# Optimization experiments

Hardware: AMD Instinct MI355X
Metric: run time of the kernel (lower is better)

The kernel has to match this reference:

```python
import jax, jax.numpy as jnp
import numpy as np

# Static config (matches init_kwargs)
B = 1
D = 1024          # model_dim
H = 16            # num_heads
HD = 64           # head_dim
TPF = 256         # tokens_per_frame = latent_height*latent_width
LH, LW = 16, 16
FRAMES = 13
PREFIX = 1
ATTN = 3
CHUNKS = 4
TXT = 226                 # text_length per chunk
SEQ_TXT = CHUNKS * TXT    # 904
VID_LEN = FRAMES * TPF    # 3328
CHUNK_VID = (PREFIX + ATTN) * TPF  # 1024 video tokens per attention chunk
THETA = 10000.0
EPS = 1e-6
SCALE = 1.0 / np.sqrt(HD)
DT, DHE, DW = 16, 24, 24  # 3D rope split of head_dim


def setup_inputs() -> dict:
    key = jax.random.key(0)
    ks = jax.random.split(key, 16)
    def w(k, shape, s=0.02):
        return (jax.random.normal(k, shape) * s).astype(jnp.float32)
    return dict(
        vid_emb=jax.random.normal(ks[0], (B, VID_LEN, D), jnp.float32),
        text_emb=jax.random.normal(ks[1], (B, SEQ_TXT, D), jnp.float32),
        Wq=w(ks[2], (D, D)), bq=jnp.zeros((D,), jnp.float32),
        Wk=w(ks[3], (D, D)), bk=jnp.zeros((D,), jnp.float32),
        Wv=w(ks[4], (D, D)), bv=jnp.zeros((D,), jnp.float32),
        Wo=w(ks[5], (D, D)), bo=jnp.zeros((D,), jnp.float32),
        qn_w=jnp.ones((HD,), jnp.float32), qn_b=jnp.zeros((HD,), jnp.float32),
        kn_w=jnp.ones((HD,), jnp.float32), kn_b=jnp.zeros((HD,), jnp.float32),
        ssm_Win=w(ks[6], (D, D)), ssm_Wout=w(ks[7], (D, D)),
        ssm_gate=jnp.zeros((D,), jnp.float32),
        fg_t=jnp.full((D,), 0.1, jnp.float32), fg_v=jnp.full((D,), 0.1, jnp.float32),
        bg_t=jnp.full((D,), 0.1, jnp.float32), bg_v=jnp.full((D,), 0.1, jnp.float32),
    )


def _layernorm(x, w, b):
    mu = jnp.mean(x, axis=-1, keepdims=True)
    var = jnp.mean((x - mu) ** 2, axis=-1, keepdims=True)
    return (x - mu) * jax.lax.rsqrt(var + EPS) * w + b


def _rope_angles():
    # per-video-token 3D positions within a chunk
    tok = jnp.arange(CHUNK_VID)
    f = (tok // TPF).astype(jnp.float32)
    rem = tok % TPF
    hp = (rem // LW).astype(jnp.float32)
    wp = (rem % LW).astype(jnp.float32)
    def inv(d):
        return THETA ** (-jnp.arange(0, d, 2, dtype=jnp.float32) / d)
    return f[:, None] * inv(DT), hp[:, None] * inv(DHE), wp[:, None] * inv(DW)


def _rot(x, ang):
    half = x.shape[-1] // 2
    c, s = jnp.cos(ang), jnp.sin(ang)
    x1, x2 = x[..., :half], x[..., half:]
    return jnp.concatenate([x1 * c - x2 * s, x1 * s + x2 * c], axis=-1)


def _apply_rope3d(x, angs):
    at, ah, aw = angs
    return jnp.concatenate([
        _rot(x[..., :DT], at),
        _rot(x[..., DT:DT + DHE], ah),
        _rot(x[..., DT + DHE:], aw),
    ], axis=-1)


def _attn_forward(vid_emb, text_emb, Wq, bq, Wk, bk, Wv, bv, Wo, bo, qn_w, qn_b, kn_w, kn_b):
    b = vid_emb.shape[0]
    starts = np.arange(CHUNKS) * ATTN * TPF
    idx = jnp.asarray(starts)[:, None] + jnp.arange(CHUNK_VID)[None, :]  # [C, CHUNK_VID]
    txt_chunks = text_emb.reshape(b, CHUNKS, TXT, D)
    vid_chunks = vid_emb[:, idx]                                          # [b, C, CHUNK_VID, D]
    cur = jnp.concatenate([txt_chunks, vid_chunks], axis=2)               # [b, C, T, D]
    T = TXT + CHUNK_VID
    cur = cur.reshape(b * CHUNKS, T, D)

    def heads(x):
        return x.reshape(b * CHUNKS, T, H, HD).transpose(0, 2, 1, 3)      # [bc, h, t, d]

    q = _layernorm(heads(cur @ Wq + bq), qn_w, qn_b)
    k = _layernorm(heads(cur @ Wk + bk), kn_w, kn_b)
    v = heads(cur @ Wv + bv)

    angs = _rope_angles()
    q = jnp.concatenate([q[:, :, :TXT], _apply_rope3d(q[:, :, TXT:], angs)], axis=2)
    k = jnp.concatenate([k[:, :, :TXT], _apply_rope3d(k[:, :, TXT:], angs)], axis=2)

    scores = jnp.einsum('bhqd,bhkd->bhqk', q, k) * SCALE
    attn = jax.nn.softmax(scores, axis=-1)
    out = jnp.einsum('bhqk,bhkd->bhqd', attn, v)
    out = out.transpose(0, 2, 1, 3).reshape(b * CHUNKS, T, D) @ Wo + bo
    out = out.reshape(b, CHUNKS, T, D)

    text_out = out[:, :, :TXT].reshape(b, SEQ_TXT, D)
    vid_part = out[:, :, TXT:]                                            # [b, C, CHUNK_VID, D]
    vid_acc = jnp.zeros((b, VID_LEN, D), vid_emb.dtype).at[:, idx].add(vid_part)
    cnt = jnp.zeros((b, VID_LEN, 1), vid_emb.dtype).at[:, idx].add(jnp.ones((b, CHUNKS, CHUNK_VID, 1), vid_emb.dtype))
    vid_out = vid_acc / cnt
    return jnp.concatenate([text_out, vid_out], axis=1)


def _ssm(x, Win, Wout, gate_logit):
    # simplified TTT stand-in: gated linear recurrence h_t = g*h_{t-1} + u_t (causal scan)
    g = jax.nn.sigmoid(gate_logit)
    u = x @ Win
    a = jnp.broadcast_to(g, u.shape)
    def comb(c1, c2):
        a1, b1 = c1
        a2, b2 = c2
        return a1 * a2, a2 * b1 + b2
    _, h = jax.lax.associative_scan(comb, (a, u), axis=1)
    return h @ Wout


def _rev_text_chunks(t):
    b = t.shape[0]
    return jnp.flip(t.reshape(b, CHUNKS, TXT, D), axis=1).reshape(b, SEQ_TXT, D)


def _ssm_forward(emb, ssm_Win, ssm_Wout, ssm_gate, fg_t, fg_v, bg_t, bg_v):
    Ttxt = SEQ_TXT
    res = emb
    y = _ssm(emb, ssm_Win, ssm_Wout, ssm_gate)
    emb = res + jnp.concatenate([jnp.tanh(fg_t) * y[:, :Ttxt], jnp.tanh(fg_v) * y[:, Ttxt:]], axis=1)
    res2 = emb
    # multiscene reverse: flip text chunk order and video token order
    rev = jnp.concatenate([_rev_text_chunks(emb[:, :Ttxt]), jnp.flip(emb[:, Ttxt:], axis=1)], axis=1)
    y2 = _ssm(rev, ssm_Win, ssm_Wout, ssm_gate)
    y2 = jnp.concatenate([_rev_text_chunks(y2[:, :Ttxt]), jnp.flip(y2[:, Ttxt:], axis=1)], axis=1)
    return res2 + jnp.concatenate([jnp.tanh(bg_t) * y2[:, :Ttxt], jnp.tanh(bg_v) * y2[:, Ttxt:]], axis=1)


def reference(vid_emb, text_emb, Wq, bq, Wk, bk, Wv, bv, Wo, bo, qn_w, qn_b, kn_w, kn_b,
              ssm_Win, ssm_Wout, ssm_gate, fg_t, fg_v, bg_t, bg_v):
    emb = _attn_forward(vid_emb, text_emb, Wq, bq, Wk, bk, Wv, bv, Wo, bo, qn_w, qn_b, kn_w, kn_b)
    out = _ssm_forward(emb, ssm_Win, ssm_Wout, ssm_gate, fg_t, fg_v, bg_t, bg_v)
    return out[:, SEQ_TXT:], out[:, :SEQ_TXT]
```

## Files before the change

kernel.cpp:

```cpp
#include <hip/hip_runtime.h>
#include <cstdint>

constexpr int Dm       = 1024;
constexpr int Hh       = 16;
constexpr int HD       = 64;
constexpr int CHUNKS   = 4;
constexpr int TXT      = 226;
constexpr int SEQ_TXT  = 904;
constexpr int VID_LEN  = 3328;
constexpr int CHUNK_VID= 1024;
constexpr int Tt       = 1250;
constexpr int Tp       = 1280;
constexpr int M_QKV    = 5000;
constexpr int SEQm     = 4232;
constexpr int STRIDE_V = 768;
constexpr float EPSc   = 1e-6f;
constexpr float SCALEc = 0.125f;
constexpr float OFFS   = 8.0f;
constexpr float C16    = 1.6609640474f;
constexpr float C24    = 1.1073093649f;

constexpr int SEGL2 = 64;
constexpr int HALO  = 64;
constexpr int NSEG2 = (SEQm + SEGL2 - 1) / SEGL2;

typedef __attribute__((ext_vector_type(8))) short bf16x8;
typedef __attribute__((ext_vector_type(4))) float f32x4;

__device__ __forceinline__ ushort f2bf(float x) {
    uint32_t u = __float_as_uint(x);
    u += 0x7FFFu + ((u >> 16) & 1u);
    return (ushort)(u >> 16);
}
__device__ __forceinline__ float bf2f(ushort b) {
    return __uint_as_float(((uint32_t)b) << 16);
}

__device__ __forceinline__ void gload_lds16(const ushort* g, ushort* l) {
    __builtin_amdgcn_global_load_lds(
        (const __attribute__((address_space(1))) unsigned int*)g,
        (__attribute__((address_space(3))) unsigned int*)l, 16, 0, 0);
}

__device__ __forceinline__ int rev_map(int i) {
    if (i < SEQ_TXT) {
        int c = i / TXT, o = i - c * TXT;
        return (CHUNKS - 1 - c) * TXT + o;
    }
    int j = i - SEQ_TXT;
    return SEQ_TXT + (VID_LEN - 1 - j);
}

__global__ __launch_bounds__(256) void prep_all(
    const float* __restrict__ Wq, const float* __restrict__ Wk,
    const float* __restrict__ Wv, const float* __restrict__ Wo,
    const float* __restrict__ Win, const float* __restrict__ Wout,
    const float* __restrict__ vid, const float* __restrict__ txt,
    ushort* __restrict__ WqkvH, ushort* __restrict__ WqkvL,
    ushort* __restrict__ WoH, ushort* __restrict__ WoL,
    ushort* __restrict__ WinH, ushort* __restrict__ WinL,
    ushort* __restrict__ WoutH, ushort* __restrict__ WoutL,
    ushort* __restrict__ chi, ushort* __restrict__ clo) {
    __shared__ float tile[32][33];
    if (blockIdx.z == 6) {
        int base = (blockIdx.y * 32 + blockIdx.x) * 256 + threadIdx.x;
        for (int idx = base; idx < M_QKV * 256; idx += 32 * 32 * 256) {
            int row = idx >> 8, c4 = (idx & 255) * 4;
            int c = row / Tt, t = row - c * Tt;
            float4 x;
            if (t < TXT)
                x = *(const float4*)(txt + (size_t)(c * TXT + t) * Dm + c4);
            else
                x = *(const float4*)(vid + (size_t)(c * STRIDE_V + (t - TXT)) * Dm + c4);
            float v[4] = {x.x, x.y, x.z, x.w};
            ushort4 h, l;
            h.x = f2bf(v[0]); l.x = f2bf(v[0] - bf2f(h.x));
            h.y = f2bf(v[1]); l.y = f2bf(v[1] - bf2f(h.y));
            h.z = f2bf(v[2]); l.z = f2bf(v[2] - bf2f(h.z));
            h.w = f2bf(v[3]); l.w = f2bf(v[3] - bf2f(h.w));
            *(ushort4*)(chi + (size_t)row * Dm + c4) = h;
            *(ushort4*)(clo + (size_t)row * Dm + c4) = l;
        }
        return;
    }
    const float* W; ushort* Thi; ushort* Tlo;
    switch (blockIdx.z) {
        case 0: W = Wq;  Thi = WqkvH;               Tlo = WqkvL;               break;
        case 1: W = Wk;  Thi = WqkvH + 1024*1024;   Tlo = WqkvL + 1024*1024;   break;
        case 2: W = Wv;  Thi = WqkvH + 2*1024*1024; Tlo = WqkvL + 2*1024*1024; break;
        case 3: W = Wo;  Thi = WoH;   Tlo = WoL;   break;
        case 4: W = Win; Thi = WinH;  Tlo = WinL;  break;
        default:W = Wout;Thi = WoutH; Tlo = WoutL; break;
    }
    int k0 = blockIdx.y * 32, n0 = blockIdx.x * 32;
    int j = threadIdx.x & 31, i0 = threadIdx.x >> 5;
#pragma unroll
    for (int i = i0; i < 32; i += 8)
        tile[i][j] = W[(size_t)(k0 + i) * 1024 + n0 + j];
    __syncthreads();
#pragma unroll
    for (int i = i0; i < 32; i += 8) {
        float v = tile[j][i];
        ushort h = f2bf(v);
        size_t o = (size_t)(n0 + i) * 1024 + k0 + j;
        Thi[o] = h;
        Tlo[o] = f2bf(v - bf2f(h));
    }
}

template<int MODE>
__global__ __launch_bounds__(256) void gemm_sk(
    const ushort* __restrict__ Ahi, const ushort* __restrict__ Alo,
    const ushort* __restrict__ Bhi, const ushort* __restrict__ Blo,
    const float* __restrict__ f1, const float* __restrict__ f2,
    const float* __restrict__ f3,
    float* __restrict__ Cf, ushort* __restrict__ u1,
    int M, int N) {
    __shared__ ushort AHL[128 * 64];
    __shared__ ushort BHL[128 * 64];
    const int tid = threadIdx.x;
    const int w = tid >> 6, lane = tid & 63;
    const int lrow = lane & 15, quad = lane >> 4;
    const int mBase = blockIdx.y * 128, nBase = blockIdx.x * 128;

    const bool isB = (w >= 2);
    const int half = w & 1;
    const ushort* Phi = isB ? Bhi : Ahi;
    const ushort* Plo = isB ? Blo : Alo;
    ushort* lds = (isB ? BHL : AHL) + half * 4096;
    const int baseR = (isB ? nBase : mBase) + half * 64;
    const int maxr = (isB ? N : M) - 1;
    const int rl8 = lane >> 3;
    const int c = (lane & 7) ^ rl8;
    const ushort* Psel = (c < 4) ? Phi : Plo;
    const ushort* gb[8];
#pragma unroll
    for (int u = 0; u < 8; ++u) {
        int rg = min(baseR + u * 8 + rl8, maxr);
        gb[u] = Psel + (size_t)rg * 1024 + (c & 3) * 8;
    }

    const int mo = (w >> 1) * 64, no = (w & 1) * 64;
    const int p = quad ^ (lrow & 7);
    f32x4 acc[4][4];
#pragma unroll
    for (int i = 0; i < 4; ++i)
#pragma unroll
        for (int j = 0; j < 4; ++j) acc[i][j] = (f32x4){0.f, 0.f, 0.f, 0.f};

    const int kk0 = (MODE == 5) ? blockIdx.z * 512 : 0;
    const int kk1 = (MODE == 5) ? kk0 + 512 : 1024;
    for (int kk = kk0; kk < kk1; kk += 32) {
        __syncthreads();
#pragma unroll
        for (int u = 0; u < 8; ++u) gload_lds16(gb[u] + kk, lds + u * 512);
        __syncthreads();

        bf16x8 ah[4], al[4], bh[4], bl[4];
#pragma unroll
        for (int i = 0; i < 4; ++i) {
            int m = mo + i * 16 + lrow;
            ah[i] = *(const bf16x8*)&AHL[m * 64 + p * 8];
            al[i] = *(const bf16x8*)&AHL[m * 64 + (p ^ 4) * 8];
        }
#pragma unroll
        for (int j = 0; j < 4; ++j) {
            int n = no + j * 16 + lrow;
            bh[j] = *(const bf16x8*)&BHL[n * 64 + p * 8];
            bl[j] = *(const bf16x8*)&BHL[n * 64 + (p ^ 4) * 8];
        }
#pragma unroll
        for (int i = 0; i < 4; ++i)
#pragma unroll
            for (int j = 0; j < 4; ++j) {
                f32x4 a = acc[i][j];
                a = __builtin_amdgcn_mfma_f32_16x16x32_bf16(ah[i], bh[j], a, 0, 0, 0);
                a = __builtin_amdgcn_mfma_f32_16x16x32_bf16(al[i], bh[j], a, 0, 0, 0);
                a = __builtin_amdgcn_mfma_f32_16x16x32_bf16(ah[i], bl[j], a, 0, 0, 0);
                acc[i][j] = a;
            }
    }

    const size_t zoff = (MODE == 5) ? (size_t)blockIdx.z * M * N : 0;
#pragma unroll
    for (int i = 0; i < 4; ++i)
#pragma unroll
        for (int j = 0; j < 4; ++j) {
            const int col = nBase + no + j * 16 + lrow;
            float bv = 0.f;
            if constexpr (MODE == 1)
                bv = (col < 1024) ? f1[col]
                   : (col < 2048) ? f2[col - 1024] : f3[col - 2048];
#pragma unroll
            for (int r = 0; r < 4; ++r) {
                const int row = mBase + mo + i * 16 + quad * 4 + r;
                if (row >= M) continue;
                const size_t idx = (size_t)row * N + col;
                const float a = acc[i][j][r];
                if constexpr (MODE == 1) {
                    u1[idx] = f2bf(a + bv);
                } else {
                    Cf[zoff + idx] = a;
                }
            }
        }
}

__global__ __launch_bounds__(512, 2) void gemm_qkv_8ph(
    const ushort* __restrict__ Ahi, const ushort* __restrict__ Alo,
    const ushort* __restrict__ Bhi, const ushort* __restrict__ Blo,
    const float* __restrict__ f1, const float* __restrict__ f2,
    const float* __restrict__ f3, ushort* __restrict__ out) {
    constexpr int Mq  = M_QKV;
    constexpr int Nq  = 3072;
    constexpr int NSL = 32;

    __shared__ __align__(16) ushort ldsq[65536];

    const int tid = threadIdx.x;
    const int w = tid >> 6, lane = tid & 63;
    const int lrow = lane & 15, quad = lane >> 4;
    const int wr = w >> 2, wc = w & 3;
    const int mBase = blockIdx.y * 256, nBase = blockIdx.x * 256;

    const int cA = (tid & 7) ^ ((tid >> 3) & 7);
    const ushort* pA = (cA < 4) ? Ahi : Alo;
    const ushort* pB = (cA < 4) ? Bhi : Blo;
    uint32_t offA[4], offB[4];
#pragma unroll
    for (int q = 0; q < 4; ++q) {
        const int r = q * 64 + (tid >> 3);
        offA[q] = (uint32_t)(min(mBase + r, Mq - 1) * 1024 + (cA & 3) * 8);
        offB[q] = (uint32_t)((nBase + r) * 1024 + (cA & 3) * 8);
    }
    const int ldsW = w * 512;

    const int pH = quad ^ (lrow & 7);
    const int arow = wr * 128 + lrow;
    const int brow = wc * 64 + lrow;

    f32x4 acc[8][4];
#pragma unroll
    for (int i = 0; i < 8; ++i)
#pragma unroll
        for (int j = 0; j < 4; ++j) acc[i][j] = (f32x4){0.f, 0.f, 0.f, 0.f};

#define STAGE_AB(b, s) do { \
        ushort* dA_ = ldsq + (b) * 16384 + ldsW; \
        ushort* dB_ = ldsq + 32768 + (b) * 16384 + ldsW; \
        const uint32_t ko_ = (uint32_t)(s) * 32u; \
        gload_lds16(pA + offA[0] + ko_, dA_); \
        gload_lds16(pA + offA[1] + ko_, dA_ + 4096); \
        gload_lds16(pA + offA[2] + ko_, dA_ + 8192); \
        gload_lds16(pA + offA[3] + ko_, dA_ + 12288); \
        gload_lds16(pB + offB[0] + ko_, dB_); \
        gload_lds16(pB + offB[1] + ko_, dB_ + 4096); \
        gload_lds16(pB + offB[2] + ko_, dB_ + 8192); \
        gload_lds16(pB + offB[3] + ko_, dB_ + 12288); \
    } while (0)

    STAGE_AB(0, 0);
    asm volatile("s_waitcnt vmcnt(0)" ::: "memory");
    __builtin_amdgcn_s_barrier();

#pragma unroll 1
    for (int s = 0; s < NSL; ++s) {
        const int b = s & 1;
        if (s + 1 < NSL) STAGE_AB(1 - b, s + 1);

        const ushort* aB_ = ldsq + b * 16384;
        const ushort* bB_ = ldsq + 32768 + b * 16384;
        bf16x8 ahi[8], alo[8], bhi[4], blo[4];
#pragma unroll
        for (int i = 0; i < 8; ++i) {
            const ushort* rp = aB_ + (arow + i * 16) * 64;
            ahi[i] = *(const bf16x8*)(rp + pH * 8);
            alo[i] = *(const bf16x8*)(rp + (pH ^ 4) * 8);
        }
#pragma unroll
        for (int j = 0; j < 4; ++j) {
            const ushort* rp = bB_ + (brow + j * 16) * 64;
            bhi[j] = *(const bf16x8*)(rp + pH * 8);
            blo[j] = *(const bf16x8*)(rp + (pH ^ 4) * 8);
        }

        __builtin_amdgcn_s_barrier();
        asm volatile("s_waitcnt lgkmcnt(0)" ::: "memory");
        __builtin_amdgcn_s_setprio(1);
#pragma unroll
        for (int i = 0; i < 8; ++i)
#pragma unroll
            for (int j = 0; j < 4; ++j) {
                f32x4 a = acc[i][j];
                a = __builtin_amdgcn_mfma_f32_16x16x32_bf16(ahi[i], bhi[j], a, 0, 0, 0);
                a = __builtin_amdgcn_mfma_f32_16x16x32_bf16(alo[i], bhi[j], a, 0, 0, 0);
                a = __builtin_amdgcn_mfma_f32_16x16x32_bf16(ahi[i], blo[j], a, 0, 0, 0);
                acc[i][j] = a;
            }
        __builtin_amdgcn_s_setprio(0);
        asm volatile("s_waitcnt vmcnt(0)" ::: "memory");
        __builtin_amdgcn_s_barrier();
    }

#undef STAGE_AB

#pragma unroll
    for (int i = 0; i < 8; ++i) {
#pragma unroll
        for (int j = 0; j < 4; ++j) {
            const int col = nBase + wc * 64 + j * 16 + lrow;
            const float bias = (col < 1024) ? f1[col]
                             : (col < 2048) ? f2[col - 1024] : f3[col - 2048];
#pragma unroll
            for (int r = 0; r < 4; ++r) {
                const int row = mBase + wr * 128 + i * 16 + quad * 4 + r;
                if (row < Mq)
                    out[(size_t)row * Nq + col] = f2bf(acc[i][j][r] + bias);
            }
        }
    }
}

__global__ __launch_bounds__(256) void lnrope(
    const ushort* __restrict__ qkvb,
    const float* __restrict__ qn_w, const float* __restrict__ qn_b,
    const float* __restrict__ kn_w, const float* __restrict__ kn_b,
    ushort* __restrict__ qP, ushort* __restrict__ kP, ushort* __restrict__ vT) {
    __shared__ ushort vtile[64][72];
    const int ch = blockIdx.y, c = ch >> 4, h = ch & 15;
    const int t0 = blockIdx.x * 64;
    const int tid = threadIdx.x, w = tid >> 6, lane = tid & 63;

    auto wsum = [](float x) {
#pragma unroll
        for (int o = 32; o; o >>= 1) x += __shfl_xor(x, o);
        return x;
    };

#pragma unroll 1
    for (int it = 0; it < 16; ++it) {
        const int tl = w * 16 + it;
        const int t = t0 + tl;
        ushort qb = 0, kb = 0, vb = 0;
        if (t < Tt) {
            size_t src = (size_t)(c * Tt + t) * 3072 + h * HD + lane;
            float qv = bf2f(qkvb[src]);
            float kv = bf2f(qkvb[src + 1024]);
            float vv = bf2f(qkvb[src + 2048]);

            float qmu = wsum(qv) * (1.f / 64.f);
            float qd  = qv - qmu;
            float qvar = wsum(qd * qd) * (1.f / 64.f);
            float qn = qd * rsqrtf(qvar + EPSc) * qn_w[lane] + qn_b[lane];

            float kmu = wsum(kv) * (1.f / 64.f);
            float kd  = kv - kmu;
            float kvar = wsum(kd * kd) * (1.f / 64.f);
            float kn = kd * rsqrtf(kvar + EPSc) * kn_w[lane] + kn_b[lane];

            if (t >= TXT) {
                int pos = t - TXT;
                int f = pos >> 8, rem2 = pos & 255, hp = rem2 >> 4, wp = rem2 & 15;
                int p, dl; float cc;
                if (lane < 16)      { cc = C16; p = f;  dl = lane; }
                else if (lane < 40) { cc = C24; p = hp; dl = lane - 16; }
                else                { cc = C24; p = wp; dl = lane - 40; }
                int halfd = (lane < 16) ? 8 : 12;
                int i = (dl < halfd) ? dl : dl - halfd;
                float ang = (float)p * exp2f(-(float)i * cc);
                float cs = cosf(ang), sn = sinf(ang);
                int partner = (dl < halfd) ? (lane + halfd) : (lane - halfd);
                float qo = __shfl(qn, partner);
                float ko = __shfl(kn, partner);
                qn = (dl < halfd) ? (qn * cs - qo * sn) : (qo * sn + qn * cs);
                kn = (dl < halfd) ? (kn * cs - ko * sn) : (ko * sn + kn * cs);
            }
            qb = f2bf(qn * SCALEc);
            kb = f2bf(kn);
            vb = f2bf(vv);
        }
        size_t dst = ((size_t)ch * Tp + t) * HD + lane;
        qP[dst] = qb;
        kP[dst] = kb;
        vtile[tl][lane] = vb;
    }
    __syncthreads();
    const int r = tid >> 2, ck = tid & 3;
    ushort* dst = vT + ((size_t)ch * HD + r) * Tp + t0;
    short o1[8], o2[8];
#pragma unroll
    for (int j = 0; j < 8; ++j) {
        o1[j] = (short)vtile[ck * 8 + j][r];
        o2[j] = (short)vtile[(ck + 4) * 8 + j][r];
    }
    *(bf16x8*)(dst + ck * 8)       = *(bf16x8*)o1;
    *(bf16x8*)(dst + (ck + 4) * 8) = *(bf16x8*)o2;
}

__global__ __launch_bounds__(256) void attn_mfma(
    const ushort* __restrict__ qP, const ushort* __restrict__ kP,
    const ushort* __restrict__ vT,
    ushort* __restrict__ ohi, ushort* __restrict__ olo) {
    const int ch = blockIdx.y;
    const int c = ch >> 4, h = ch & 15;
    const int qbase = blockIdx.x * 64;
    const int tid = threadIdx.x, w = tid >> 6, lane = tid & 63;
    const int lrow = lane & 15, quad = lane >> 4;

    __shared__ ushort KT[2][32 * 64];
    __shared__ ushort VTs[2][64 * 32];
    __shared__ ushort PB[4][16][40];

    const ushort* kg = kP + (size_t)ch * Tp * HD;
    const ushort* vg = vT + (size_t)ch * HD * Tp;

    const ushort* kgl = kg + (size_t)(w * 8 + (lane >> 3)) * HD
                           + ((lane & 7) ^ ((lane >> 3) & 7)) * 8;
    const ushort* vgl = vg + (size_t)(w * 16 + (lane >> 2)) * Tp + (lane & 3) * 8;

    const int qr = qbase + w * 16 + lrow;
    const ushort* qgp = qP + ((size_t)ch * Tp + qr) * HD + quad * 8;
    bf16x8 qf0 = *(const bf16x8*)qgp;
    bf16x8 qf1 = *(const bf16x8*)(qgp + 32);

    f32x4 accO[4];
#pragma unroll
    for (int dt = 0; dt < 4; ++dt) accO[dt] = (f32x4){0.f, 0.f, 0.f, 0.f};
    float lacc[4] = {0.f, 0.f, 0.f, 0.f};

    gload_lds16(kgl, &KT[0][w * 512]);
    gload_lds16(vgl, &VTs[0][w * 512]);

    const int NSTEP = Tp / 32;
    for (int s = 0; s < NSTEP; ++s) {
        const int b = s & 1;
        __syncthreads();
        if (s + 1 < NSTEP) {
            int kb = (s + 1) * 32;
            gload_lds16(kgl + (size_t)kb * HD, &KT[1 - b][w * 512]);
            gload_lds16(vgl + kb, &VTs[1 - b][w * 512]);
        }

        const int sw = lrow & 7;
        const ushort* r0 = &KT[b][lrow * 64];
        const ushort* r1 = &KT[b][(16 + lrow) * 64];
        bf16x8 k00 = *(const bf16x8*)(r0 + (quad ^ sw) * 8);
        bf16x8 k01 = *(const bf16x8*)(r0 + ((4 + quad) ^ sw) * 8);
        bf16x8 k10 = *(const bf16x8*)(r1 + (quad ^ sw) * 8);
        bf16x8 k11 = *(const bf16x8*)(r1 + ((4 + quad) ^ sw) * 8);
        f32x4 s0 = (f32x4){0.f, 0.f, 0.f, 0.f}, s1 = s0;
        s0 = __builtin_amdgcn_mfma_f32_16x16x32_bf16(qf0, k00, s0, 0, 0, 0);
        s0 = __builtin_amdgcn_mfma_f32_16x16x32_bf16(qf1, k01, s0, 0, 0, 0);
        s1 = __builtin_amdgcn_mfma_f32_16x16x32_bf16(qf0, k10, s1, 0, 0, 0);
        s1 = __builtin_amdgcn_mfma_f32_16x16x32_bf16(qf1, k11, s1, 0, 0, 0);

#pragma unroll
        for (int r = 0; r < 4; ++r) {
            float p0 = __expf(s0[r] - OFFS);
            float p1 = __expf(s1[r] - OFFS);
            lacc[r] += p0 + p1;
            int row = quad * 4 + r;
            PB[w][row][lrow]      = f2bf(p0);
            PB[w][row][16 + lrow] = f2bf(p1);
        }

        bf16x8 pf = *(const bf16x8*)&PB[w][lrow][quad * 8];
#pragma unroll
        for (int dt = 0; dt < 4; ++dt) {
            bf16x8 vf = *(const bf16x8*)&VTs[b][(dt * 16 + lrow) * 32 + quad * 8];
            accO[dt] = __builtin_amdgcn_mfma_f32_16x16x32_bf16(pf, vf, accO[dt], 0, 0, 0);
        }
    }

    float il[4];
#pragma unroll
    for (int r = 0; r < 4; ++r) {
        float l = lacc[r];
        l += __shfl_xor(l, 1);
        l += __shfl_xor(l, 2);
        l += __shfl_xor(l, 4);
        l += __shfl_xor(l, 8);
        l -= (float)(Tp - Tt) * __expf(-OFFS);
        il[r] = 1.f / l;
    }
#pragma unroll
    for (int dt = 0; dt < 4; ++dt)
#pragma unroll
        for (int r = 0; r < 4; ++r) {
            int qrow = qbase + w * 16 + quad * 4 + r;
            if (qrow < Tt) {
                float val = accO[dt][r] * il[r];
                size_t o = (size_t)(c * Tt + qrow) * Dm + h * HD + dt * 16 + lrow;
                ushort hv = f2bf(val);
                ohi[o] = hv;
                olo[o] = f2bf(val - bf2f(hv));
            }
        }
}

__global__ __launch_bounds__(256) void reduce_scatter(
    const float* __restrict__ P0, const float* __restrict__ bo,
    ushort* __restrict__ ehi, ushort* __restrict__ elo) {
    const float* P1 = P0 + (size_t)M_QKV * Dm;
    int idx = blockIdx.x * 256 + threadIdx.x;
    int row = idx >> 8, c4 = (idx & 255) * 4;
    float sx, sy, sz, sw;
    if (row < SEQ_TXT) {
        int c = row / TXT, t = row - c * TXT;
        size_t o = (size_t)(c * Tt + t) * Dm + c4;
        float4 a = *(const float4*)(P0 + o);
        float4 b = *(const float4*)(P1 + o);
        sx = a.x + b.x; sy = a.y + b.y; sz = a.z + b.z; sw = a.w + b.w;
    } else {
        int p = row - SEQ_TXT;
        sx = sy = sz = sw = 0.f; int cnt = 0;
#pragma unroll
        for (int c = 0; c < CHUNKS; ++c) {
            int off = p - c * STRIDE_V;
            if (off >= 0 && off < CHUNK_VID) {
                size_t o = (size_t)(c * Tt + TXT + off) * Dm + c4;
                float4 a = *(const float4*)(P0 + o);
                float4 b = *(const float4*)(P1 + o);
                sx += a.x + b.x; sy += a.y + b.y;
                sz += a.z + b.z; sw += a.w + b.w;
                ++cnt;
            }
        }
        float inv = 1.f / (float)cnt;
        sx *= inv; sy *= inv; sz *= inv; sw *= inv;
    }
    float4 b4 = *(const float4*)(bo + c4);
    float v[4] = {sx + b4.x, sy + b4.y, sz + b4.z, sw + b4.w};
    ushort4 h, l;
    h.x = f2bf(v[0]); l.x = f2bf(v[0] - bf2f(h.x));
    h.y = f2bf(v[1]); l.y = f2bf(v[1] - bf2f(h.y));
    h.z = f2bf(v[2]); l.z = f2bf(v[2] - bf2f(h.z));
    h.w = f2bf(v[3]); l.w = f2bf(v[3] - bf2f(h.w));
    *(ushort4*)(ehi + (size_t)row * Dm + c4) = h;
    *(ushort4*)(elo + (size_t)row * Dm + c4) = l;
}

__global__ __launch_bounds__(256) void scan_halo(
    const float* __restrict__ P0, const float* __restrict__ gate,
    ushort* __restrict__ hhi, ushort* __restrict__ hlo, int perm) {
    const float* P1 = P0 + (size_t)SEQm * Dm;
    int ch = blockIdx.x * 256 + threadIdx.x;
    int seg = blockIdx.y;
    float g = 1.f / (1.f + expf(-gate[ch]));
    int tw0 = seg * SEGL2;
    int tw1 = min(SEQm, tw0 + SEGL2);
    int t0 = max(0, tw0 - HALO);
    float hv = 0.f;
    for (int t = t0; t < tw0; ++t) {
        int rt = perm ? rev_map(t) : t;
        size_t o = (size_t)rt * Dm + ch;
        hv = fmaf(g, hv, P0[o] + P1[o]);
    }
    for (int t = tw0; t < tw1; ++t) {
        int rt = perm ? rev_map(t) : t;
        size_t o = (size_t)rt * Dm + ch;
        hv = fmaf(g, hv, P0[o] + P1[o]);
        ushort h = f2bf(hv);
        hhi[o] = h;
        hlo[o] = f2bf(hv - bf2f(h));
    }
}

__global__ __launch_bounds__(256) void reduce_c1(
    const float* __restrict__ P0,
    const ushort* __restrict__ ehi, const ushort* __restrict__ elo,
    const float* __restrict__ fg_t, const float* __restrict__ fg_v,
    float* __restrict__ emb2, ushort* __restrict__ e2hi, ushort* __restrict__ e2lo) {
    const float* P1 = P0 + (size_t)SEQm * Dm;
    int idx = blockIdx.x * 256 + threadIdx.x;
    int row = idx >> 8, c4 = (idx & 255) * 4;
    const float* fg = (row < SEQ_TXT) ? fg_t : fg_v;
    size_t o = (size_t)row * Dm + c4;
    float4 a = *(const float4*)(P0 + o);
    float4 b = *(const float4*)(P1 + o);
    ushort4 eh = *(const ushort4*)(ehi + o);
    ushort4 el = *(const ushort4*)(elo + o);
    float v[4];
    v[0] = (bf2f(eh.x) + bf2f(el.x)) + tanhf(fg[c4 + 0]) * (a.x + b.x);
    v[1] = (bf2f(eh.y) + bf2f(el.y)) + tanhf(fg[c4 + 1]) * (a.y + b.y);
    v[2] = (bf2f(eh.z) + bf2f(el.z)) + tanhf(fg[c4 + 2]) * (a.z + b.z);
    v[3] = (bf2f(eh.w) + bf2f(el.w)) + tanhf(fg[c4 + 3]) * (a.w + b.w);
    *(float4*)(emb2 + o) = make_float4(v[0], v[1], v[2], v[3]);
    ushort4 h, l;
    h.x = f2bf(v[0]); l.x = f2bf(v[0] - bf2f(h.x));
    h.y = f2bf(v[1]); l.y = f2bf(v[1] - bf2f(h.y));
    h.z = f2bf(v[2]); l.z = f2bf(v[2] - bf2f(h.z));
    h.w = f2bf(v[3]); l.w = f2bf(v[3] - bf2f(h.w));
    *(ushort4*)(e2hi + o) = h;
    *(ushort4*)(e2lo + o) = l;
}

__global__ __launch_bounds__(256) void reduce_fin(
    const float* __restrict__ P0, const float* __restrict__ emb2,
    const float* __restrict__ bg_t, const float* __restrict__ bg_v,
    float* __restrict__ outp) {
    const float* P1 = P0 + (size_t)SEQm * Dm;
    int idx = blockIdx.x * 256 + threadIdx.x;
    int row = idx >> 8, c4 = (idx & 255) * 4;
    const float* bg = (row < SEQ_TXT) ? bg_t : bg_v;
    int drow = (row >= SEQ_TXT) ? (row - SEQ_TXT) : (VID_LEN + row);
    size_t o = (size_t)row * Dm + c4;
    float4 a = *(const float4*)(P0 + o);
    float4 b = *(const float4*)(P1 + o);
    float4 e = *(const float4*)(emb2 + o);
    float4 r = make_float4(e.x + tanhf(bg[c4 + 0]) * (a.x + b.x),
                           e.y + tanhf(bg[c4 + 1]) * (a.y + b.y),
                           e.z + tanhf(bg[c4 + 2]) * (a.z + b.z),
                           e.w + tanhf(bg[c4 + 3]) * (a.w + b.w));
    *(float4*)(outp + (size_t)drow * Dm + c4) = r;
}

extern "C" void kernel_launch(void* const* d_in, const int* in_sizes, int n_in,
                              void* d_out, int out_size, void* d_ws, size_t ws_size,
                              hipStream_t stream) {
    const float* vid_emb = (const float*)d_in[0];
    const float* text_emb= (const float*)d_in[1];
    const float* Wq = (const float*)d_in[2];  const float* bq = (const float*)d_in[3];
    const float* Wk = (const float*)d_in[4];  const float* bk = (const float*)d_in[5];
    const float* Wv = (const float*)d_in[6];  const float* bv = (const float*)d_in[7];
    const float* Wo = (const float*)d_in[8];  const float* bo = (const float*)d_in[9];
    const float* qn_w = (const float*)d_in[10]; const float* qn_b = (const float*)d_in[11];
    const float* kn_w = (const float*)d_in[12]; const float* kn_b = (const float*)d_in[13];
    const float* Win  = (const float*)d_in[14]; const float* Wout = (const float*)d_in[15];
    const float* gate = (const float*)d_in[16];
    const float* fg_t = (const float*)d_in[17]; const float* fg_v = (const float*)d_in[18];
    const float* bg_t = (const float*)d_in[19]; const float* bg_v = (const float*)d_in[20];

    char* W8 = (char*)d_ws;
    if (ws_size < 128647168u) return;
    ushort* WqkvH = (ushort*)(W8 + 0);
    ushort* WqkvL = (ushort*)(W8 + 6291456);
    ushort* WoH   = (ushort*)(W8 + 12582912);
    ushort* WoL   = (ushort*)(W8 + 14680064);
    ushort* WinH  = (ushort*)(W8 + 16777216);
    ushort* WinL  = (ushort*)(W8 + 18874368);
    ushort* WoutH = (ushort*)(W8 + 20971520);
    ushort* WoutL = (ushort*)(W8 + 23068672);
    ushort* qkvb  = (ushort*)(W8 + 25165824);
    ushort* curH  = (ushort*)(W8 + 55885824);
    ushort* curL  = (ushort*)(W8 + 66125824);
    ushort* qPl   = (ushort*)(W8 + 76365824);
    ushort* kPl   = (ushort*)(W8 + 86851584);
    ushort* vTl   = (ushort*)(W8 + 97337344);
    ushort* aoutH = (ushort*)(W8 + 25165824);
    ushort* aoutL = (ushort*)(W8 + 35405824);
    float*  PWo   = (float*) (W8 + 76365824);
    ushort* embH  = (ushort*)(W8 + 45645824);
    ushort* embL  = (ushort*)(W8 + 54312960);
    float*  PW    = (float*) (W8 + 76365824);
    ushort* hbufH = (ushort*)(W8 + 25165824);
    ushort* hbufL = (ushort*)(W8 + 33832960);
    float*  emb2  = (float*) (W8 + 111034368);
    ushort* e2H   = (ushort*)(W8 + 25165824);
    ushort* e2L   = (ushort*)(W8 + 33832960);
    ushort* hbuf2H= (ushort*)(W8 + 45645824);
    ushort* hbuf2L= (ushort*)(W8 + 54312960);
    float*  outp  = (float*)d_out;

    prep_all<<<dim3(32, 32, 7), 256, 0, stream>>>(
        Wq, Wk, Wv, Wo, Win, Wout, vid_emb, text_emb,
        WqkvH, WqkvL, WoH, WoL, WinH, WinL, WoutH, WoutL, curH, curL);

    gemm_qkv_8ph<<<dim3(12, 20), 512, 0, stream>>>(
        curH, curL, WqkvH, WqkvL, bq, bk, bv, qkvb);

    lnrope<<<dim3(Tp / 64, 64), 256, 0, stream>>>(qkvb, qn_w, qn_b, kn_w, kn_b,
                                                  qPl, kPl, vTl);

    attn_mfma<<<dim3(Tp / 64, 64), 256, 0, stream>>>(qPl, kPl, vTl, aoutH, aoutL);

    gemm_sk<5><<<dim3(8, 40, 2), 256, 0, stream>>>(
        aoutH, aoutL, WoH, WoL, nullptr, nullptr, nullptr, PWo, nullptr,
        M_QKV, 1024);
    reduce_scatter<<<SEQm, 256, 0, stream>>>(PWo, bo, embH, embL);

    dim3 gsq(8, 34, 2);
    dim3 gscan(Dm / 256, NSEG2);

    gemm_sk<5><<<gsq, 256, 0, stream>>>(
        embH, embL, WinH, WinL, nullptr, nullptr, nullptr, PW, nullptr,
        SEQm, 1024);
    scan_halo<<<gscan, 256, 0, stream>>>(PW, gate, hbufH, hbufL, 0);
    gemm_sk<5><<<gsq, 256, 0, stream>>>(
        hbufH, hbufL, WoutH, WoutL, nullptr, nullptr, nullptr, PW, nullptr,
        SEQm, 1024);
    reduce_c1<<<SEQm, 256, 0, stream>>>(PW, embH, embL, fg_t, fg_v,
                                        emb2, e2H, e2L);

    gemm_sk<5><<<gsq, 256, 0, stream>>>(
        e2H, e2L, WinH, WinL, nullptr, nullptr, nullptr, PW, nullptr,
        SEQm, 1024);
    scan_halo<<<gscan, 256, 0, stream>>>(PW, gate, hbuf2H, hbuf2L, 1);
    gemm_sk<5><<<gsq, 256, 0, stream>>>(
        hbuf2H, hbuf2L, WoutH, WoutL, nullptr, nullptr, nullptr, PW, nullptr,
        SEQm, 1024);
    reduce_fin<<<SEQm, 256, 0, stream>>>(PW, emb2, bg_t, bg_v, outp);
}
```

Before: 656.5 us.

## Double-buffer LDS tiles in split-bf16 GEMM to overlap loads with MFMA

Doubles the LDS staging buffers in the gemm_sk kernel so the next k-slice is fetched directly into LDS while MFMAs run on the current slice. This replaces the two barriers per iteration with one wait-and-barrier at the end. It also raises wave priority around the MFMA block. LDS use doubles to 64 KB per block, which may cut occupancy.

```diff
diff --git a/kernel.cpp b/kernel.cpp
--- a/kernel.cpp
+++ b/kernel.cpp
@@ -116,8 +116,8 @@
     const float* __restrict__ f3,
     float* __restrict__ Cf, ushort* __restrict__ u1,
     int M, int N) {
-    __shared__ ushort AHL[128 * 64];
-    __shared__ ushort BHL[128 * 64];
+    __shared__ ushort AHL[2][128 * 64];
+    __shared__ ushort BHL[2][128 * 64];
     const int tid = threadIdx.x;
     const int w = tid >> 6, lane = tid & 63;
     const int lrow = lane & 15, quad = lane >> 4;
@@ -127,7 +127,8 @@
     const int half = w & 1;
     const ushort* Phi = isB ? Bhi : Ahi;
     const ushort* Plo = isB ? Blo : Alo;
-    ushort* lds = (isB ? BHL : AHL) + half * 4096;
+    ushort* st0 = (isB ? BHL[0] : AHL[0]) + half * 4096;
+    ushort* st1 = (isB ? BHL[1] : AHL[1]) + half * 4096;
     const int baseR = (isB ? nBase : mBase) + half * 64;
     const int maxr = (isB ? N : M) - 1;
     const int rl8 = lane >> 3;
@@ -150,25 +151,37 @@
 
     const int kk0 = (MODE == 5) ? blockIdx.z * 512 : 0;
     const int kk1 = (MODE == 5) ? kk0 + 512 : 1024;
-    for (int kk = kk0; kk < kk1; kk += 32) {
-        __syncthreads();
-#pragma unroll
-        for (int u = 0; u < 8; ++u) gload_lds16(gb[u] + kk, lds + u * 512);
-        __syncthreads();
-
+
+#pragma unroll
+    for (int u = 0; u < 8; ++u) gload_lds16(gb[u] + kk0, st0 + u * 512);
+    asm volatile("s_waitcnt vmcnt(0)" ::: "memory");
+    __builtin_amdgcn_s_barrier();
+
+    int it = 0;
+    for (int kk = kk0; kk < kk1; kk += 32, ++it) {
+        const int b = it & 1;
+        ushort* stN = b ? st0 : st1;
+        if (kk + 32 < kk1) {
+#pragma unroll
+            for (int u = 0; u < 8; ++u) gload_lds16(gb[u] + kk + 32, stN + u * 512);
+        }
+
+        const ushort* Ab = AHL[b];
+        const ushort* Bb = BHL[b];
         bf16x8 ah[4], al[4], bh[4], bl[4];
 #pragma unroll
         for (int i = 0; i < 4; ++i) {
             int m = mo + i * 16 + lrow;
-            ah[i] = *(const bf16x8*)&AHL[m * 64 + p * 8];
-            al[i] = *(const bf16x8*)&AHL[m * 64 + (p ^ 4) * 8];
+            ah[i] = *(const bf16x8*)&Ab[m * 64 + p * 8];
+            al[i] = *(const bf16x8*)&Ab[m * 64 + (p ^ 4) * 8];
         }
 #pragma unroll
         for (int j = 0; j < 4; ++j) {
             int n = no + j * 16 + lrow;
-            bh[j] = *(const bf16x8*)&BHL[n * 64 + p * 8];
-            bl[j] = *(const bf16x8*)&BHL[n * 64 + (p ^ 4) * 8];
-        }
+            bh[j] = *(const bf16x8*)&Bb[n * 64 + p * 8];
+            bl[j] = *(const bf16x8*)&Bb[n * 64 + (p ^ 4) * 8];
+        }
+        __builtin_amdgcn_s_setprio(1);
 #pragma unroll
         for (int i = 0; i < 4; ++i)
 #pragma unroll
@@ -179,6 +192,9 @@
                 a = __builtin_amdgcn_mfma_f32_16x16x32_bf16(ah[i], bl[j], a, 0, 0, 0);
                 acc[i][j] = a;
             }
+        __builtin_amdgcn_s_setprio(0);
+        asm volatile("s_waitcnt vmcnt(0)" ::: "memory");
+        __builtin_amdgcn_s_barrier();
     }
 
     const size_t zoff = (MODE == 5) ? (size_t)blockIdx.z * M * N : 0;
```

New measurement: 647.2 us. Within noise of the previous version (-1.4%).
